# Kernel optimization log

Measured on AMD Instinct MI355X. Metric: run time of the kernel, lower is better.

## Reference

```python
import jax, jax.numpy as jnp
import numpy as np

N = 100000      # nodes
E = 1600000     # edges
D_IN = 128      # input_dim
H = 256         # hidden_dim
L = 3           # num_layers
B = 64          # graphs per batch
BN_EPS = 1e-5


def setup_inputs() -> dict:
    key = jax.random.key(0)
    ks = jax.random.split(key, 8)
    x = jax.random.normal(ks[0], (N, D_IN), dtype=jnp.float32)
    edge_index = jax.random.randint(ks[1], (2, E), 0, N, dtype=jnp.int32)
    batch = jnp.sort(jax.random.randint(ks[2], (N,), 0, B, dtype=jnp.int32))
    W0 = jax.random.normal(ks[3], (D_IN, H), dtype=jnp.float32) / np.sqrt(D_IN)
    W_rest = jax.random.normal(ks[4], (L - 1, H, H), dtype=jnp.float32) / np.sqrt(H)
    b = jax.random.normal(ks[5], (L, H), dtype=jnp.float32) * 0.01
    gamma = 1.0 + jax.random.normal(ks[6], (L, H), dtype=jnp.float32) * 0.01
    beta = jax.random.normal(ks[7], (L, H), dtype=jnp.float32) * 0.01
    return {"x": x, "W0": W0, "W_rest": W_rest, "b": b, "gamma": gamma,
            "beta": beta, "edge_index": edge_index, "batch": batch}


def reference(x, W0, W_rest, b, gamma, beta, edge_index, batch):
    src, dst = edge_index[0], edge_index[1]
    # GCN symmetric normalization with self-loops: deg = in-degree + 1
    deg = jax.ops.segment_sum(jnp.ones((E,), x.dtype), dst, num_segments=N) + 1.0
    dis = jax.lax.rsqrt(deg)                   # deg^{-1/2}, [N]
    enorm = dis[src] * dis[dst]                # per-edge norm, [E]
    self_norm = (dis * dis)[:, None]           # self-loop norm = 1/deg, [N,1]

    def gcn_bn_relu(h, W, bb, g, be):
        h = h @ W                                                  # [N,H]
        agg = jax.ops.segment_sum(h[src] * enorm[:, None], dst, num_segments=N)
        h = agg + h * self_norm + bb                               # self-loop + bias
        # BatchNorm1d (training mode: batch stats, biased variance)
        m = h.mean(axis=0)
        v = h.var(axis=0)
        h = (h - m) * jax.lax.rsqrt(v + BN_EPS) * g + be
        return jax.nn.relu(h)                                      # dropout = identity (eval)

    h = gcn_bn_relu(x, W0, b[0], gamma[0], beta[0])
    for i in range(L - 1):
        h = gcn_bn_relu(h, W_rest[i], b[i + 1], gamma[i + 1], beta[i + 1])

    # segment pooling per graph (att_pool in the original is dead code: not returned)
    counts = jax.ops.segment_sum(jnp.ones((N,), h.dtype), batch, num_segments=B)
    mean_pool = jax.ops.segment_sum(h, batch, num_segments=B) / counts[:, None]
    max_pool = jax.ops.segment_max(h, batch, num_segments=B)
    return jnp.concatenate([mean_pool, max_pool], axis=1)          # [B, 2H]
```

## Files before the change

kernel.cpp:

```cpp
#include <hip/hip_runtime.h>
#include <hip/hip_bf16.h>
#include <stdint.h>


#define NN 100000
#define EE 1600000
#define BB 64
#define MPAD 100096
#define NBM (MPAD / 256)

typedef __attribute__((ext_vector_type(8))) short short8;
typedef __attribute__((ext_vector_type(4))) float f32x4;

__device__ __forceinline__ float bflo(uint32_t v){ return __uint_as_float(v << 16); }
__device__ __forceinline__ float bfhi(uint32_t v){ return __uint_as_float(v & 0xffff0000u); }
__device__ __forceinline__ uint32_t bfrne(float x){
  uint32_t u = __float_as_uint(x);
  return (u + 0x7fffu + ((u >> 16) & 1u)) >> 16;
}
__device__ __forceinline__ uint32_t bfpack(float a, float b){ return bfrne(a) | (bfrne(b) << 16); }
__device__ __forceinline__ float phi(long long p){
  return __uint_as_float((uint32_t)((unsigned long long)p >> 32));
}

__device__ __forceinline__ void gload_lds16(const void* g, void* l){
  __builtin_amdgcn_global_load_lds(
      (const __attribute__((address_space(1))) uint32_t*)g,
      (__attribute__((address_space(3))) uint32_t*)l, 16, 0, 0);
}

__global__ void k_deg(const int* __restrict__ dst, int* __restrict__ degi){
  for (int e = blockIdx.x * blockDim.x + threadIdx.x; e < EE; e += gridDim.x * blockDim.x)
    atomicAdd(&degi[dst[e]], 1);
}

__global__ void k_scan1(const int* __restrict__ degi, int* __restrict__ rp, int* __restrict__ bsum,
                        float* __restrict__ dis){
  __shared__ int lds[256];
  int b = blockIdx.x, t = threadIdx.x;
  int base = b * 1024 + t * 4;
  int v0 = (base + 0 < NN) ? degi[base + 0] : 0;
  int v1 = (base + 1 < NN) ? degi[base + 1] : 0;
  int v2 = (base + 2 < NN) ? degi[base + 2] : 0;
  int v3 = (base + 3 < NN) ? degi[base + 3] : 0;
  if (base + 0 < NN) dis[base + 0] = rsqrtf((float)v0 + 1.0f);
  if (base + 1 < NN) dis[base + 1] = rsqrtf((float)v1 + 1.0f);
  if (base + 2 < NN) dis[base + 2] = rsqrtf((float)v2 + 1.0f);
  if (base + 3 < NN) dis[base + 3] = rsqrtf((float)v3 + 1.0f);
  int s = v0 + v1 + v2 + v3;
  lds[t] = s; __syncthreads();
  for (int off = 1; off < 256; off <<= 1){
    int x = (t >= off) ? lds[t - off] : 0; __syncthreads();
    lds[t] += x; __syncthreads();
  }
  int excl = lds[t] - s;
  if (t == 255) bsum[b] = lds[255];
  if (base + 0 < NN) rp[base + 0] = excl;
  if (base + 1 < NN) rp[base + 1] = excl + v0;
  if (base + 2 < NN) rp[base + 2] = excl + v0 + v1;
  if (base + 3 < NN) rp[base + 3] = excl + v0 + v1 + v2;
}

__global__ void k_scan2(int* __restrict__ bsum, int nb){
  if (blockIdx.x == 0 && threadIdx.x == 0){
    int run = 0;
    for (int i = 0; i < nb; ++i){ int t = bsum[i]; bsum[i] = run; run += t; }
  }
}

__global__ void k_scan3(int* __restrict__ rp, int* __restrict__ cursor, const int* __restrict__ bsum){
  int b = blockIdx.x, t = threadIdx.x;
  int add = bsum[b];
  int base = b * 1024 + t * 4;
  #pragma unroll
  for (int j = 0; j < 4; ++j){
    int i = base + j;
    if (i < NN){ int v = rp[i] + add; rp[i] = v; cursor[i] = v; }
  }
  if (b == 0 && t == 0) rp[NN] = EE;
}

__global__ void k_fill(const int* __restrict__ src, const int* __restrict__ dst,
                       const float* __restrict__ dis, int* __restrict__ cursor,
                       long long* __restrict__ cp){
  for (int e = blockIdx.x * blockDim.x + threadIdx.x; e < EE; e += gridDim.x * blockDim.x){
    int s = src[e], d = dst[e];
    int pos = atomicAdd(&cursor[d], 1);
    float nrm = dis[s] * dis[d];
    long long v = (long long)(unsigned int)s | ((long long)(unsigned int)__float_as_uint(nrm) << 32);
    cp[pos] = v;
  }
}

__global__ void k_sort(const int* __restrict__ rp, long long* __restrict__ cp){
  int wid = (blockIdx.x * blockDim.x + threadIdx.x) >> 6;
  int lane = threadIdx.x & 63;
  if (wid >= NN) return;
  int beg = rp[wid], end = rp[wid + 1];
  int d = end - beg;
  if (d <= 1) return;
  if (d <= 64){
    long long key = (lane < d) ? cp[beg + lane] : 0x7fffffffffffffffLL;
    #pragma unroll
    for (int k = 2; k <= 64; k <<= 1){
      #pragma unroll
      for (int j = k >> 1; j > 0; j >>= 1){
        long long other = __shfl_xor(key, j);
        bool up = ((lane & k) == 0);
        bool keepMin = (((lane & j) == 0) == up);
        bool take = keepMin ? (other < key) : (other > key);
        if (take) key = other;
      }
    }
    if (lane < d) cp[beg + lane] = key;
  } else if (lane == 0){
    for (int i = beg + 1; i < end; ++i){
      long long k2 = cp[i];
      int j = i - 1;
      while (j >= beg && cp[j] > k2){ cp[j + 1] = cp[j]; --j; }
      cp[j + 1] = k2;
    }
  }
}

__global__ void k_wtall(const float* __restrict__ W0, const float* __restrict__ Wr,
                        uint16_t* __restrict__ Wt0, uint16_t* __restrict__ Wt1,
                        uint16_t* __restrict__ Wt2){
  int i = blockIdx.x * 256 + threadIdx.x;
  if (i < 32768){
    int c = i >> 7, k = i & 127;
    Wt0[i] = (uint16_t)bfrne(W0[k * 256 + c]);
  } else if (i < 32768 + 131072){
    int j = i - 32768;
    int m = j >> 16, jj = j & 65535;
    int c = jj >> 8, k = jj & 255;
    uint16_t v = (uint16_t)bfrne(Wr[m * 65536 + k * 256 + c]);
    if (m == 0) Wt1[jj] = v; else Wt2[jj] = v;
  }
}

__global__ void k_cvtx(const float* __restrict__ x, uint32_t* __restrict__ Xb){
  int i = blockIdx.x * 256 + threadIdx.x;
  if (i >= MPAD * 64) return;
  int row = i >> 6;
  uint32_t r = 0u;
  if (row < NN){
    int col = (i & 63) * 2;
    r = bfpack(x[row * 128 + col], x[row * 128 + col + 1]);
  }
  Xb[i] = r;
}

__global__ void k_agg256(const uint2* __restrict__ Xin, const int* __restrict__ rp,
                         const long long* __restrict__ cp, const float* __restrict__ dis,
                         uint2* __restrict__ Xout){
  const uint2* C2 = (const uint2*)cp;
  int lane = threadIdx.x & 63;
  int slot = threadIdx.x >> 6;
  int g8 = lane & 56;
  int row0 = blockIdx.x * 16 + slot;
  for (int rr = 0; rr < 4; ++rr){
    int row = row0 + rr * 4;
    if (row >= NN){
      if (row < MPAD){ uint2 z = {0u, 0u}; Xout[(size_t)row * 64 + lane] = z; }
      continue;
    }
    int beg = rp[row], end = rp[row + 1];
    int nf = (end - beg) >> 3;
    float a0 = 0.f, a1 = 0.f, a2 = 0.f, a3 = 0.f;
    uint2 cA = {0u,0u}, cB = {0u,0u};
    uint2 vA[8], vB[8];

    if (nf > 0){
      cA = C2[beg + (lane & 7)];
      #pragma unroll
      for (int u = 0; u < 8; ++u){
        int su = __shfl((int)cA.x, g8 | u);
        vA[u] = Xin[(size_t)su * 64 + lane];
      }
    }
    if (nf > 1){
      cB = C2[beg + 8 + (lane & 7)];
      #pragma unroll
      for (int u = 0; u < 8; ++u){
        int su = __shfl((int)cB.x, g8 | u);
        vB[u] = Xin[(size_t)su * 64 + lane];
      }
    }

#define CONSUME(c, v) { \
    _Pragma("unroll") \
    for (int u = 0; u < 8; ++u){ \
      float w = __uint_as_float((uint32_t)__shfl((int)c.y, g8 | u)); \
      a0 += w * bflo(v[u].x); a1 += w * bfhi(v[u].x); \
      a2 += w * bflo(v[u].y); a3 += w * bfhi(v[u].y); \
    } }
#define REFILL(c, v, pk) if ((pk) < nf){ \
    c = C2[beg + (pk) * 8 + (lane & 7)]; \
    _Pragma("unroll") \
    for (int u = 0; u < 8; ++u){ \
      int su = __shfl((int)c.x, g8 | u); \
      v[u] = Xin[(size_t)su * 64 + lane]; \
    } }

    int it = 0;
    while (it + 1 < nf){
      CONSUME(cA, vA); REFILL(cA, vA, it + 2);
      CONSUME(cB, vB); REFILL(cB, vB, it + 3);
      it += 2;
    }
    if (it < nf){ CONSUME(cA, vA); ++it; }
#undef CONSUME
#undef REFILL

    for (int e = beg + nf * 8; e < end; ++e){
      long long p0 = cp[e];
      float w = phi(p0);
      uint2 v = Xin[(size_t)(int)p0 * 64 + lane];
      a0 += w * bflo(v.x); a1 += w * bfhi(v.x);
      a2 += w * bflo(v.y); a3 += w * bfhi(v.y);
    }
    float dv = dis[row]; float sn = dv * dv;
    uint2 vs = Xin[(size_t)row * 64 + lane];
    a0 += sn * bflo(vs.x); a1 += sn * bfhi(vs.x);
    a2 += sn * bflo(vs.y); a3 += sn * bfhi(vs.y);
    uint2 o; o.x = bfpack(a0, a1); o.y = bfpack(a2, a3);
    Xout[(size_t)row * 64 + lane] = o;
  }
}

__global__ void k_agg128(const uint2* __restrict__ Xin, const int* __restrict__ rp,
                         const long long* __restrict__ cp, const float* __restrict__ dis,
                         uint2* __restrict__ Xout){
  int lane = threadIdx.x & 63;
  int half = lane >> 5, j = lane & 31;
  int slot = threadIdx.x >> 6;
  int row0 = blockIdx.x * 16 + slot;
  for (int rr = 0; rr < 4; ++rr){
    int row = row0 + rr * 4;
    if (row >= NN){
      if (row < MPAD && half == 0){ uint2 z = {0u, 0u}; Xout[(size_t)row * 32 + j] = z; }
      continue;
    }
    int beg = rp[row], end = rp[row + 1];
    float a0 = 0.f, a1 = 0.f, a2 = 0.f, a3 = 0.f;
    int e = beg;
    for (; e + 8 <= end; e += 8){
      long long p[4]; uint2 v[4];
      #pragma unroll
      for (int u = 0; u < 4; ++u) p[u] = cp[e + u * 2 + half];
      #pragma unroll
      for (int u = 0; u < 4; ++u) v[u] = Xin[(size_t)(int)p[u] * 32 + j];
      #pragma unroll
      for (int u = 0; u < 4; ++u){
        float w = phi(p[u]);
        a0 += w * bflo(v[u].x); a1 += w * bfhi(v[u].x);
        a2 += w * bflo(v[u].y); a3 += w * bfhi(v[u].y);
      }
    }
    for (; e < end; e += 2){
      int idx = e + half;
      bool ok = idx < end;
      long long p0 = cp[ok ? idx : end - 1];
      float w = ok ? phi(p0) : 0.f;
      uint2 v = Xin[(size_t)(int)p0 * 32 + j];
      a0 += w * bflo(v.x); a1 += w * bfhi(v.x);
      a2 += w * bflo(v.y); a3 += w * bfhi(v.y);
    }
    a0 += __shfl_xor(a0, 32); a1 += __shfl_xor(a1, 32);
    a2 += __shfl_xor(a2, 32); a3 += __shfl_xor(a3, 32);
    if (half == 0){
      float dv = dis[row]; float sn = dv * dv;
      uint2 vs = Xin[(size_t)row * 32 + j];
      a0 += sn * bflo(vs.x); a1 += sn * bfhi(vs.x);
      a2 += sn * bflo(vs.y); a3 += sn * bfhi(vs.y);
      uint2 o; o.x = bfpack(a0, a1); o.y = bfpack(a2, a3);
      Xout[(size_t)row * 32 + j] = o;
    }
  }
}

template<int K>
__global__ __launch_bounds__(512) void k_gemm(const uint16_t* __restrict__ A,
                                              const uint16_t* __restrict__ Bt,
                                              uint32_t* __restrict__ Cb,
                                              float* __restrict__ pstat){
  __shared__ __align__(16) uint16_t lA[2][8192];
  __shared__ __align__(16) uint16_t lB[2][4096];
  __shared__ float lp[8][128];
  int tid = threadIdx.x;
  int l = tid & 63;
  int bm = blockIdx.x, bn = blockIdx.y;

  f32x4 acc[4][4];
  #pragma unroll
  for (int m = 0; m < 4; ++m)
    #pragma unroll
    for (int n = 0; n < 4; ++n){ f32x4 z = {0.f,0.f,0.f,0.f}; acc[m][n] = z; }

  int w = tid >> 6, wr = w >> 1, wc = w & 1;
  int rbase = wr * 64, cbase = wc * 64;
  int lrow = l & 15, lk8 = l >> 4;

  auto stage = [&](int kt, int buf){
    #pragma unroll
    for (int i = 0; i < 2; ++i){
      int c = i * 512 + tid;
      int k8 = c >> 8, r = c & 255;
      size_t ga = (size_t)(bm * 256 + r) * K + kt * 32 + k8 * 8;
      gload_lds16((const char*)(A + ga), (char*)&lA[buf][c * 8]);
    }
    int k8b = tid >> 7, rb = tid & 127;
    size_t gb = (size_t)(bn * 128 + rb) * K + kt * 32 + k8b * 8;
    gload_lds16((const char*)(Bt + gb), (char*)&lB[buf][tid * 8]);
  };

  stage(0, 0);
  __syncthreads();
  constexpr int NT = K / 32;
  for (int kt = 0; kt < NT; ++kt){
    int cur = kt & 1;
    if (kt + 1 < NT) stage(kt + 1, cur ^ 1);
    short8 afr[4], bfr[4];
    #pragma unroll
    for (int m = 0; m < 4; ++m)
      afr[m] = *(const short8*)&lA[cur][(lk8 * 256 + rbase + m * 16 + lrow) * 8];
    #pragma unroll
    for (int n = 0; n < 4; ++n)
      bfr[n] = *(const short8*)&lB[cur][(lk8 * 128 + cbase + n * 16 + lrow) * 8];
    #pragma unroll
    for (int m = 0; m < 4; ++m)
      #pragma unroll
      for (int n = 0; n < 4; ++n)
        acc[m][n] = __builtin_amdgcn_mfma_f32_16x16x32_bf16(afr[m], bfr[n], acc[m][n], 0, 0, 0);
    __syncthreads();
  }

  int grow0 = bm * 256 + rbase + (l >> 4) * 4;
  int gcol0 = bn * 128 + cbase + (l & 15);
  uint16_t* C16 = (uint16_t*)Cb;
  float sa[4] = {0.f,0.f,0.f,0.f}, sb[4] = {0.f,0.f,0.f,0.f};
  #pragma unroll
  for (int m = 0; m < 4; ++m){
    #pragma unroll
    for (int n = 0; n < 4; ++n){
      int col = gcol0 + n * 16;
      int r0 = grow0 + m * 16;
      f32x4 v = acc[m][n];
      #pragma unroll
      for (int q = 0; q < 4; ++q){
        C16[(size_t)(r0 + q) * 256 + col] = (uint16_t)bfrne(v[q]);
        sa[n] += v[q]; sb[n] += v[q] * v[q];
      }
    }
  }
  #pragma unroll
  for (int n = 0; n < 4; ++n){
    sa[n] += __shfl_xor(sa[n], 16); sa[n] += __shfl_xor(sa[n], 32);
    sb[n] += __shfl_xor(sb[n], 16); sb[n] += __shfl_xor(sb[n], 32);
  }
  if (l < 16){
    #pragma unroll
    for (int n = 0; n < 4; ++n){
      lp[w][n * 16 + l] = sa[n];
      lp[w][64 + n * 16 + l] = sb[n];
    }
  }
  __syncthreads();
  if (tid < 256){
    int kind = tid >> 7, c = tid & 127;
    int wc2 = c >> 6, cc = c & 63;
    float v = lp[wc2][kind * 64 + cc] + lp[2 + wc2][kind * 64 + cc]
            + lp[4 + wc2][kind * 64 + cc] + lp[6 + wc2][kind * 64 + cc];
    pstat[(size_t)(bm * 2 + bn) * 256 + kind * 128 + c] = v;
  }
}

__global__ void k_finalize(const float* __restrict__ pstat, const float* __restrict__ gamma,
                           const float* __restrict__ beta, float* __restrict__ ss){
  int c = threadIdx.x;
  int bn = c >> 7, lc = c & 127;
  double s[8], s2[8];
  #pragma unroll
  for (int j = 0; j < 8; ++j){ s[j] = 0.; s2[j] = 0.; }
  int bm = 0;
  for (; bm + 8 <= NBM; bm += 8){
    #pragma unroll
    for (int j = 0; j < 8; ++j){
      const float* p = pstat + (size_t)((bm + j) * 2 + bn) * 256;
      s[j]  += (double)p[lc];
      s2[j] += (double)p[128 + lc];
    }
  }
  for (; bm < NBM; ++bm){
    const float* p = pstat + (size_t)(bm * 2 + bn) * 256;
    s[0]  += (double)p[lc];
    s2[0] += (double)p[128 + lc];
  }
  double S  = ((s[0]+s[1])+(s[2]+s[3]))  + ((s[4]+s[5])+(s[6]+s[7]));
  double S2 = ((s2[0]+s2[1])+(s2[2]+s2[3])) + ((s2[4]+s2[5])+(s2[6]+s2[7]));
  double mean = S / (double)NN;
  double var  = S2 / (double)NN - mean * mean;
  float rstd = rsqrtf((float)var + 1e-5f);
  float sc = gamma[c] * rstd;
  ss[c] = sc;
  ss[256 + c] = beta[c] - (float)mean * sc;
}

__global__ void k_bnapply(const uint4* __restrict__ Y, const float* __restrict__ ss,
                          uint4* __restrict__ X){
  int i = blockIdx.x * 256 + threadIdx.x;
  if (i >= MPAD * 32) return;
  uint4 v = Y[i];
  int c0 = (i & 31) * 8;
  float r0 = fmaxf(bflo(v.x) * ss[c0 + 0] + ss[256 + c0 + 0], 0.f);
  float r1 = fmaxf(bfhi(v.x) * ss[c0 + 1] + ss[256 + c0 + 1], 0.f);
  float r2 = fmaxf(bflo(v.y) * ss[c0 + 2] + ss[256 + c0 + 2], 0.f);
  float r3 = fmaxf(bfhi(v.y) * ss[c0 + 3] + ss[256 + c0 + 3], 0.f);
  float r4 = fmaxf(bflo(v.z) * ss[c0 + 4] + ss[256 + c0 + 4], 0.f);
  float r5 = fmaxf(bfhi(v.z) * ss[c0 + 5] + ss[256 + c0 + 5], 0.f);
  float r6 = fmaxf(bflo(v.w) * ss[c0 + 6] + ss[256 + c0 + 6], 0.f);
  float r7 = fmaxf(bfhi(v.w) * ss[c0 + 7] + ss[256 + c0 + 7], 0.f);
  uint4 o;
  o.x = bfpack(r0, r1); o.y = bfpack(r2, r3);
  o.z = bfpack(r4, r5); o.w = bfpack(r6, r7);
  X[i] = o;
}

__device__ __forceinline__ int segfind(const int* __restrict__ batch, int g){
  if (g <= 0) return 0;
  if (g >= BB) return NN;
  int lo = 0, hi = NN;
  while (lo < hi){ int mid = (lo + hi) >> 1; if (batch[mid] < g) lo = mid + 1; else hi = mid; }
  return lo;
}

__global__ void k_poolpart(const uint32_t* __restrict__ X, const int* __restrict__ batch,
                           float* __restrict__ pb){
  int g = blockIdx.x, c = blockIdx.y, t = threadIdx.x;
  int s = segfind(batch, g), e = segfind(batch, g + 1);
  int len = e - s;
  int c0 = s + (int)(((long long)len * c) >> 3);
  int c1 = s + (int)(((long long)len * (c + 1)) >> 3);
  float sm0 = 0.f, sm1 = 0.f, mx0 = -1e30f, mx1 = -1e30f;
  #pragma unroll 4
  for (int r = c0; r < c1; ++r){
    uint32_t v = X[(size_t)r * 128 + t];
    float a = bflo(v), b2 = bfhi(v);
    sm0 += a; sm1 += b2;
    mx0 = fmaxf(mx0, a); mx1 = fmaxf(mx1, b2);
  }
  float* p = pb + (size_t)(g * 8 + c) * 512;
  p[2 * t] = sm0; p[2 * t + 1] = sm1;
  p[256 + 2 * t] = mx0; p[256 + 2 * t + 1] = mx1;
}

__global__ void k_poolred(const float* __restrict__ pb, const int* __restrict__ batch,
                          float* __restrict__ out){
  int g = blockIdx.x, cc = threadIdx.x;
  float s = 0.f, m = -1e30f;
  #pragma unroll
  for (int c = 0; c < 8; ++c){
    const float* p = pb + (size_t)(g * 8 + c) * 512;
    s += p[cc];
    m = fmaxf(m, p[256 + cc]);
  }
  float inv = 1.0f / (float)(segfind(batch, g + 1) - segfind(batch, g));
  out[g * 512 + cc] = s * inv;
  out[g * 512 + 256 + cc] = m;
}

extern "C" void kernel_launch(void* const* d_in, const int* in_sizes, int n_in,
                              void* d_out, int out_size, void* d_ws, size_t ws_size,
                              hipStream_t stream){
  const float* x     = (const float*)d_in[0];
  const float* W0    = (const float*)d_in[1];
  const float* Wr    = (const float*)d_in[2];
  const float* gamma = (const float*)d_in[4];
  const float* beta  = (const float*)d_in[5];
  const int*   ei    = (const int*)d_in[6];
  const int*   batch = (const int*)d_in[7];
  const int* esrc = ei;
  const int* edst = ei + EE;
  float* out = (float*)d_out;

  char* base = (char*)d_ws;
  size_t off = 0;
  auto alloc = [&](size_t b)->char*{
    char* p = base + off; off = (off + b + 255) & ~(size_t)255; return p;
  };
  uint32_t* Xbuf = (uint32_t*)alloc((size_t)MPAD * 256 * 2);
  uint32_t* Xagg = (uint32_t*)alloc((size_t)MPAD * 256 * 2);
  uint32_t* Y    = (uint32_t*)alloc((size_t)MPAD * 256 * 2);
  uint16_t* Wt0  = (uint16_t*)alloc(256 * 128 * 2);
  uint16_t* Wt1  = (uint16_t*)alloc(256 * 256 * 2);
  uint16_t* Wt2  = (uint16_t*)alloc(256 * 256 * 2);
  int*   degi   = (int*)  alloc((size_t)NN * 4);
  float* dis    = (float*)alloc((size_t)NN * 4);
  int*   rp     = (int*)  alloc((size_t)(NN + 1) * 4);
  int*   cursor = (int*)  alloc((size_t)NN * 4);
  int*   bsum   = (int*)  alloc(128 * 4);
  long long* cp = (long long*)alloc((size_t)EE * 8);
  float* pstat  = (float*)alloc((size_t)NBM * 2 * 256 * 4);
  float* ss     = (float*)alloc(512 * 4);
  float* pb     = (float*)alloc((size_t)BB * 8 * 512 * 4);

  hipMemsetAsync(degi, 0, (size_t)NN * 4, stream);
  k_deg<<<2048, 256, 0, stream>>>(edst, degi);
  k_scan1<<<98, 256, 0, stream>>>(degi, rp, bsum, dis);
  k_scan2<<<1, 1, 0, stream>>>(bsum, 98);
  k_scan3<<<98, 256, 0, stream>>>(rp, cursor, bsum);
  k_fill<<<2048, 256, 0, stream>>>(esrc, edst, dis, cursor, cp);
  k_sort<<<NN / 4, 256, 0, stream>>>(rp, cp);
  k_wtall<<<640, 256, 0, stream>>>(W0, Wr, Wt0, Wt1, Wt2);
  k_cvtx<<<MPAD * 64 / 256, 256, 0, stream>>>(x, Xbuf);

  k_agg128<<<MPAD / 16, 256, 0, stream>>>((const uint2*)Xbuf, rp, cp, dis, (uint2*)Xagg);
  k_gemm<128><<<dim3(NBM, 2), 512, 0, stream>>>((const uint16_t*)Xagg, Wt0, Y, pstat);
  k_finalize<<<1, 256, 0, stream>>>(pstat, gamma + 0, beta + 0, ss);
  k_bnapply<<<MPAD * 32 / 256, 256, 0, stream>>>((const uint4*)Y, ss, (uint4*)Xbuf);

  k_agg256<<<MPAD / 16, 256, 0, stream>>>((const uint2*)Xbuf, rp, cp, dis, (uint2*)Xagg);
  k_gemm<256><<<dim3(NBM, 2), 512, 0, stream>>>((const uint16_t*)Xagg, Wt1, Y, pstat);
  k_finalize<<<1, 256, 0, stream>>>(pstat, gamma + 256, beta + 256, ss);
  k_bnapply<<<MPAD * 32 / 256, 256, 0, stream>>>((const uint4*)Y, ss, (uint4*)Xbuf);

  k_agg256<<<MPAD / 16, 256, 0, stream>>>((const uint2*)Xbuf, rp, cp, dis, (uint2*)Xagg);
  k_gemm<256><<<dim3(NBM, 2), 512, 0, stream>>>((const uint16_t*)Xagg, Wt2, Y, pstat);
  k_finalize<<<1, 256, 0, stream>>>(pstat, gamma + 512, beta + 512, ss);
  k_bnapply<<<MPAD * 32 / 256, 256, 0, stream>>>((const uint4*)Y, ss, (uint4*)Xbuf);

  k_poolpart<<<dim3(BB, 8), 128, 0, stream>>>(Xbuf, batch, pb);
  k_poolred<<<BB, 256, 0, stream>>>(pb, batch, out);
}
```

Before: 868.8 us.

## Fuse prep kernels, fold final BN into pooling, simplify agg256, add nontemporal hints

Merges the weight-transpose and x-conversion kernels into one launch. Drops the last BN-apply pass by applying scale, shift and ReLU inside the pooling kernel, which reads Y directly. Replaces agg256's shuffle-based double-buffered edge pipeline with a plain 8-wide unrolled loop. Adds nontemporal loads and stores for the CSR entries and the aggregation outputs. The simpler agg loop may hide less memory latency, and nontemporal stores may push Xagg out of cache before the GEMM reads it.

```diff
diff --git a/kernel.cpp b/kernel.cpp
--- a/kernel.cpp
+++ b/kernel.cpp
@@ -123,98 +123,67 @@
   }
 }
 
-__global__ void k_wtall(const float* __restrict__ W0, const float* __restrict__ Wr,
-                        uint16_t* __restrict__ Wt0, uint16_t* __restrict__ Wt1,
-                        uint16_t* __restrict__ Wt2){
-  int i = blockIdx.x * 256 + threadIdx.x;
-  if (i < 32768){
-    int c = i >> 7, k = i & 127;
-    Wt0[i] = (uint16_t)bfrne(W0[k * 256 + c]);
-  } else if (i < 32768 + 131072){
-    int j = i - 32768;
-    int m = j >> 16, jj = j & 65535;
-    int c = jj >> 8, k = jj & 255;
-    uint16_t v = (uint16_t)bfrne(Wr[m * 65536 + k * 256 + c]);
-    if (m == 0) Wt1[jj] = v; else Wt2[jj] = v;
-  }
-}
-
-__global__ void k_cvtx(const float* __restrict__ x, uint32_t* __restrict__ Xb){
-  int i = blockIdx.x * 256 + threadIdx.x;
-  if (i >= MPAD * 64) return;
-  int row = i >> 6;
-  uint32_t r = 0u;
-  if (row < NN){
-    int col = (i & 63) * 2;
-    r = bfpack(x[row * 128 + col], x[row * 128 + col + 1]);
-  }
-  Xb[i] = r;
+__global__ void k_prep(const float* __restrict__ W0, const float* __restrict__ Wr,
+                       uint16_t* __restrict__ Wt0, uint16_t* __restrict__ Wt1,
+                       uint16_t* __restrict__ Wt2,
+                       const float* __restrict__ x, uint32_t* __restrict__ Xb){
+  int b = blockIdx.x;
+  if (b < 640){
+    int i = b * 256 + threadIdx.x;
+    if (i < 32768){
+      int c = i >> 7, k = i & 127;
+      Wt0[i] = (uint16_t)bfrne(W0[k * 256 + c]);
+    } else if (i < 32768 + 131072){
+      int j = i - 32768;
+      int m = j >> 16, jj = j & 65535;
+      int c = jj >> 8, k = jj & 255;
+      uint16_t v = (uint16_t)bfrne(Wr[m * 65536 + k * 256 + c]);
+      if (m == 0) Wt1[jj] = v; else Wt2[jj] = v;
+    }
+  } else {
+    int i = (b - 640) * 256 + threadIdx.x;
+    if (i >= MPAD * 64) return;
+    int row = i >> 6;
+    uint32_t r = 0u;
+    if (row < NN){
+      int col = (i & 63) * 2;
+      r = bfpack(x[row * 128 + col], x[row * 128 + col + 1]);
+    }
+    Xb[i] = r;
+  }
 }
 
 __global__ void k_agg256(const uint2* __restrict__ Xin, const int* __restrict__ rp,
                          const long long* __restrict__ cp, const float* __restrict__ dis,
                          uint2* __restrict__ Xout){
-  const uint2* C2 = (const uint2*)cp;
   int lane = threadIdx.x & 63;
   int slot = threadIdx.x >> 6;
-  int g8 = lane & 56;
   int row0 = blockIdx.x * 16 + slot;
   for (int rr = 0; rr < 4; ++rr){
     int row = row0 + rr * 4;
     if (row >= NN){
-      if (row < MPAD){ uint2 z = {0u, 0u}; Xout[(size_t)row * 64 + lane] = z; }
+      if (row < MPAD)
+        __builtin_nontemporal_store(0ull, (unsigned long long*)&Xout[(size_t)row * 64 + lane]);
       continue;
     }
     int beg = rp[row], end = rp[row + 1];
-    int nf = (end - beg) >> 3;
     float a0 = 0.f, a1 = 0.f, a2 = 0.f, a3 = 0.f;
-    uint2 cA = {0u,0u}, cB = {0u,0u};
-    uint2 vA[8], vB[8];
-
-    if (nf > 0){
-      cA = C2[beg + (lane & 7)];
+    int e = beg;
+    for (; e + 8 <= end; e += 8){
+      long long p[8]; uint2 v[8];
+      #pragma unroll
+      for (int u = 0; u < 8; ++u) p[u] = __builtin_nontemporal_load(&cp[e + u]);
+      #pragma unroll
+      for (int u = 0; u < 8; ++u) v[u] = Xin[(size_t)(int)p[u] * 64 + lane];
       #pragma unroll
       for (int u = 0; u < 8; ++u){
-        int su = __shfl((int)cA.x, g8 | u);
-        vA[u] = Xin[(size_t)su * 64 + lane];
+        float w = phi(p[u]);
+        a0 += w * bflo(v[u].x); a1 += w * bfhi(v[u].x);
+        a2 += w * bflo(v[u].y); a3 += w * bfhi(v[u].y);
       }
     }
-    if (nf > 1){
-      cB = C2[beg + 8 + (lane & 7)];
-      #pragma unroll
-      for (int u = 0; u < 8; ++u){
-        int su = __shfl((int)cB.x, g8 | u);
-        vB[u] = Xin[(size_t)su * 64 + lane];
-      }
-    }
-
-#define CONSUME(c, v) { \
-    _Pragma("unroll") \
-    for (int u = 0; u < 8; ++u){ \
-      float w = __uint_as_float((uint32_t)__shfl((int)c.y, g8 | u)); \
-      a0 += w * bflo(v[u].x); a1 += w * bfhi(v[u].x); \
-      a2 += w * bflo(v[u].y); a3 += w * bfhi(v[u].y); \
-    } }
-#define REFILL(c, v, pk) if ((pk) < nf){ \
-    c = C2[beg + (pk) * 8 + (lane & 7)]; \
-    _Pragma("unroll") \
-    for (int u = 0; u < 8; ++u){ \
-      int su = __shfl((int)c.x, g8 | u); \
-      v[u] = Xin[(size_t)su * 64 + lane]; \
-    } }
-
-    int it = 0;
-    while (it + 1 < nf){
-      CONSUME(cA, vA); REFILL(cA, vA, it + 2);
-      CONSUME(cB, vB); REFILL(cB, vB, it + 3);
-      it += 2;
-    }
-    if (it < nf){ CONSUME(cA, vA); ++it; }
-#undef CONSUME
-#undef REFILL
-
-    for (int e = beg + nf * 8; e < end; ++e){
-      long long p0 = cp[e];
+    for (; e < end; ++e){
+      long long p0 = __builtin_nontemporal_load(&cp[e]);
       float w = phi(p0);
       uint2 v = Xin[(size_t)(int)p0 * 64 + lane];
       a0 += w * bflo(v.x); a1 += w * bfhi(v.x);
@@ -224,8 +193,9 @@
     uint2 vs = Xin[(size_t)row * 64 + lane];
     a0 += sn * bflo(vs.x); a1 += sn * bfhi(vs.x);
     a2 += sn * bflo(vs.y); a3 += sn * bfhi(vs.y);
-    uint2 o; o.x = bfpack(a0, a1); o.y = bfpack(a2, a3);
-    Xout[(size_t)row * 64 + lane] = o;
+    unsigned long long o = (unsigned long long)bfpack(a0, a1)
+                         | ((unsigned long long)bfpack(a2, a3) << 32);
+    __builtin_nontemporal_store(o, (unsigned long long*)&Xout[(size_t)row * 64 + lane]);
   }
 }
 
@@ -239,7 +209,8 @@
   for (int rr = 0; rr < 4; ++rr){
     int row = row0 + rr * 4;
     if (row >= NN){
-      if (row < MPAD && half == 0){ uint2 z = {0u, 0u}; Xout[(size_t)row * 32 + j] = z; }
+      if (row < MPAD && half == 0)
+        __builtin_nontemporal_store(0ull, (unsigned long long*)&Xout[(size_t)row * 32 + j]);
       continue;
     }
     int beg = rp[row], end = rp[row + 1];
@@ -248,7 +219,7 @@
     for (; e + 8 <= end; e += 8){
       long long p[4]; uint2 v[4];
       #pragma unroll
-      for (int u = 0; u < 4; ++u) p[u] = cp[e + u * 2 + half];
+      for (int u = 0; u < 4; ++u) p[u] = __builtin_nontemporal_load(&cp[e + u * 2 + half]);
       #pragma unroll
       for (int u = 0; u < 4; ++u) v[u] = Xin[(size_t)(int)p[u] * 32 + j];
       #pragma unroll
@@ -274,8 +245,9 @@
       uint2 vs = Xin[(size_t)row * 32 + j];
       a0 += sn * bflo(vs.x); a1 += sn * bfhi(vs.x);
       a2 += sn * bflo(vs.y); a3 += sn * bfhi(vs.y);
-      uint2 o; o.x = bfpack(a0, a1); o.y = bfpack(a2, a3);
-      Xout[(size_t)row * 32 + j] = o;
+      unsigned long long o = (unsigned long long)bfpack(a0, a1)
+                           | ((unsigned long long)bfpack(a2, a3) << 32);
+      __builtin_nontemporal_store(o, (unsigned long long*)&Xout[(size_t)row * 32 + j]);
     }
   }
 }
@@ -435,9 +407,11 @@
   return lo;
 }
 
-__global__ void k_poolpart(const uint32_t* __restrict__ X, const int* __restrict__ batch,
-                           float* __restrict__ pb){
+__global__ void k_poolpart(const uint32_t* __restrict__ Y, const float* __restrict__ ss,
+                           const int* __restrict__ batch, float* __restrict__ pb){
   int g = blockIdx.x, c = blockIdx.y, t = threadIdx.x;
+  float sc0 = ss[2*t], sc1 = ss[2*t+1];
+  float sh0 = ss[256+2*t], sh1 = ss[256+2*t+1];
   int s = segfind(batch, g), e = segfind(batch, g + 1);
   int len = e - s;
   int c0 = s + (int)(((long long)len * c) >> 3);
@@ -445,8 +419,9 @@
   float sm0 = 0.f, sm1 = 0.f, mx0 = -1e30f, mx1 = -1e30f;
   #pragma unroll 4
   for (int r = c0; r < c1; ++r){
-    uint32_t v = X[(size_t)r * 128 + t];
-    float a = bflo(v), b2 = bfhi(v);
+    uint32_t v = Y[(size_t)r * 128 + t];
+    float a  = fmaxf(bflo(v) * sc0 + sh0, 0.f);
+    float b2 = fmaxf(bfhi(v) * sc1 + sh1, 0.f);
     sm0 += a; sm1 += b2;
     mx0 = fmaxf(mx0, a); mx1 = fmaxf(mx1, b2);
   }
@@ -512,8 +487,7 @@
   k_scan3<<<98, 256, 0, stream>>>(rp, cursor, bsum);
   k_fill<<<2048, 256, 0, stream>>>(esrc, edst, dis, cursor, cp);
   k_sort<<<NN / 4, 256, 0, stream>>>(rp, cp);
-  k_wtall<<<640, 256, 0, stream>>>(W0, Wr, Wt0, Wt1, Wt2);
-  k_cvtx<<<MPAD * 64 / 256, 256, 0, stream>>>(x, Xbuf);
+  k_prep<<<640 + MPAD * 64 / 256, 256, 0, stream>>>(W0, Wr, Wt0, Wt1, Wt2, x, Xbuf);
 
   k_agg128<<<MPAD / 16, 256, 0, stream>>>((const uint2*)Xbuf, rp, cp, dis, (uint2*)Xagg);
   k_gemm<128><<<dim3(NBM, 2), 512, 0, stream>>>((const uint16_t*)Xagg, Wt0, Y, pstat);
@@ -528,8 +502,7 @@
   k_agg256<<<MPAD / 16, 256, 0, stream>>>((const uint2*)Xbuf, rp, cp, dis, (uint2*)Xagg);
   k_gemm<256><<<dim3(NBM, 2), 512, 0, stream>>>((const uint16_t*)Xagg, Wt2, Y, pstat);
   k_finalize<<<1, 256, 0, stream>>>(pstat, gamma + 512, beta + 512, ss);
-  k_bnapply<<<MPAD * 32 / 256, 256, 0, stream>>>((const uint4*)Y, ss, (uint4*)Xbuf);
-
-  k_poolpart<<<dim3(BB, 8), 128, 0, stream>>>(Xbuf, batch, pb);
+
+  k_poolpart<<<dim3(BB, 8), 128, 0, stream>>>(Y, ss, batch, pb);
   k_poolred<<<BB, 256, 0, stream>>>(pb, batch, out);
 }
```

Measured after the change: 849.9 us. -2.2%, faster.
